# Performance work log

Hardware: AMD Instinct MI355X
Metric: run time of the kernel (lower is better)

## Reference

```python
import jax, jax.numpy as jnp
import numpy as np

NUM_SAMPLES = 1024


def _cdist(a, b):
    # a, b: (n, 3) -> (n, n) pairwise euclidean distances (torch.cdist p=2)
    d2 = jnp.sum((a[:, None, :] - b[None, :, :]) ** 2, axis=-1)
    return jnp.sqrt(jnp.maximum(d2, 0.0))


def _greedy_match_cost(cost):
    # Greedy sequential matching: repeatedly take the global argmin over
    # still-unmatched rows/cols, accumulate its cost, eliminate row+col.
    n = cost.shape[0]

    def step(carry, _):
        row_mask, col_mask, loss = carry
        valid = row_mask[:, None] & col_mask[None, :]
        masked = jnp.where(valid, cost, jnp.inf)
        idx = jnp.argmin(masked)  # row-major first-min == torch's min(dim=1)+argmin tiebreak
        r = idx // n
        c = idx % n
        loss = loss + cost[r, c]
        return (row_mask.at[r].set(False), col_mask.at[c].set(False), loss), None

    init = (jnp.ones((n,), dtype=bool), jnp.ones((n,), dtype=bool), jnp.float32(0.0))
    (_, _, loss), _ = jax.lax.scan(step, init, None, length=n)
    return loss / n


def setup_inputs() -> dict:
    key = jax.random.key(0)
    k1, k2, k3 = jax.random.split(key, 3)
    B, N, n = 8, 4096, NUM_SAMPLES
    S1 = jax.random.normal(k1, (B, N, 3), dtype=jnp.float32)
    S2 = jax.random.normal(k2, (B, N, 3), dtype=jnp.float32)
    # torch.randperm(N)[:n] per batch element: without-replacement sampling
    perm_keys = jax.random.split(k3, B)
    indices = jax.vmap(lambda k: jax.random.permutation(k, N)[:n])(perm_keys).astype(jnp.int32)
    return {"S1": S1, "S2": S2, "indices": indices}


def reference(S1, S2, indices):
    # sample the same indices from both sets, per batch (matches original loop)
    s1 = jnp.take_along_axis(S1, indices[:, :, None], axis=1)  # (B, n, 3)
    s2 = jnp.take_along_axis(S2, indices[:, :, None], axis=1)  # (B, n, 3)
    cost = jax.vmap(_cdist)(s1, s2)  # (B, n, n)
    losses = jax.vmap(_greedy_match_cost)(cost)  # (B,)
    return jnp.mean(losses)
```

## Files before the change

kernel.cpp:

```cpp
#include <hip/hip_runtime.h>
#include <stdint.h>

#define BATCH 8
#define NPTS 4096
#define NS 1024
#define KD 6

typedef unsigned long long u64;
typedef unsigned int u32;
typedef unsigned short u16;
typedef unsigned char u8;

#define DEADV (~0ull)
#define QNANB 0x7FC00000u

__device__ __forceinline__ float pdist3(float ax, float ay, float az,
                                        float bx, float by, float bz) {
    float dx = ax - bx, dy = ay - by, dz = az - bz;
    float d2 = __fmaf_rn(dz, dz, __fmaf_rn(dy, dy, dx * dx));
    return __fsqrt_rn(d2);
}

__device__ __forceinline__ u64 packv(float d, u32 row, u32 col) {
    return ((u64)__float_as_uint(d) << 20) | ((u64)row << 10) | (u64)col;
}

__device__ __forceinline__ u64 u64min2(u64 a, u64 b) { return a < b ? a : b; }
__device__ __forceinline__ u64 u64max2(u64 a, u64 b) { return a > b ? a : b; }

__device__ __forceinline__ u64 tree16(const u64* p) {
    u64 a0 = u64min2(p[0], p[1]),   a1 = u64min2(p[2], p[3]);
    u64 a2 = u64min2(p[4], p[5]),   a3 = u64min2(p[6], p[7]);
    u64 a4 = u64min2(p[8], p[9]),   a5 = u64min2(p[10], p[11]);
    u64 a6 = u64min2(p[12], p[13]), a7 = u64min2(p[14], p[15]);
    u64 b0 = u64min2(a0, a1), b1 = u64min2(a2, a3);
    u64 b2 = u64min2(a4, a5), b3 = u64min2(a6, a7);
    return u64min2(u64min2(b0, b1), u64min2(b2, b3));
}

template<int CTRL>
__device__ __forceinline__ u64 dpp_min_step(u64 m) {
    u32 lo = (u32)m, hi = (u32)(m >> 32);
    u32 olo = (u32)__builtin_amdgcn_update_dpp(-1, (int)lo, CTRL, 0xF, 0xF, false);
    u32 ohi = (u32)__builtin_amdgcn_update_dpp(-1, (int)hi, CTRL, 0xF, 0xF, false);
    u64 o = ((u64)ohi << 32) | olo;
    return o < m ? o : m;
}

__device__ __forceinline__ u64 wave_min_u64(u64 m) {
    m = dpp_min_step<0x111>(m);
    m = dpp_min_step<0x112>(m);
    m = dpp_min_step<0x114>(m);
    m = dpp_min_step<0x118>(m);
    m = dpp_min_step<0x142>(m);
    m = dpp_min_step<0x143>(m);
    u32 lo = (u32)__builtin_amdgcn_readlane((int)(u32)m, 63);
    u32 hi = (u32)__builtin_amdgcn_readlane((int)(u32)(m >> 32), 63);
    return ((u64)hi << 32) | lo;
}

__global__ void gather_k(const float* __restrict__ S1, const float* __restrict__ S2,
                         const int* __restrict__ idx,
                         float4* __restrict__ s1g, float4* __restrict__ s2g,
                         int* __restrict__ cnt) {
    int t = blockIdx.x * blockDim.x + threadIdx.x;
    if (t == 0) *cnt = 0;
    if (t >= BATCH * NS) return;
    int b = t >> 10;
    int j = idx[t];
    const float* p1 = S1 + ((size_t)b * NPTS + j) * 3;
    const float* p2 = S2 + ((size_t)b * NPTS + j) * 3;
    s1g[t] = make_float4(p1[0], p1[1], p1[2], 0.f);
    s2g[t] = make_float4(p2[0], p2[1], p2[2], 0.f);
}

__global__ void lists_k(const float4* __restrict__ s1g, const float4* __restrict__ s2g,
                        u64* __restrict__ rlist_g, u64* __restrict__ clist_g) {
    int gg = blockIdx.x * 4 + (threadIdx.x >> 6);
    int lane = threadIdx.x & 63;
    int side = (gg >= BATCH * NS) ? 1 : 0;
    int g = gg - side * (BATCH * NS);
    int b = g >> 10;
    u32 rc = (u32)(g & 1023);
    float4 a = side ? s2g[g] : s1g[g];
    const float4* other = (side ? s1g : s2g) + (size_t)b * NS;
    u64 cand[16];
    #pragma unroll
    for (int k = 0; k < 16; ++k) {
        int o = lane + (k << 6);
        float4 q = other[o];
        float d = pdist3(a.x, a.y, a.z, q.x, q.y, q.z);
        cand[k] = side ? packv(d, (u32)o, rc) : packv(d, rc, (u32)o);
    }
    u64* out = (side ? clist_g : rlist_g) + (size_t)g * KD;
    for (int i = 0; i < KD; ++i) {
        u64 m1 = wave_min_u64(tree16(cand));
        if (lane == 0) out[i] = m1;
        #pragma unroll
        for (int k = 0; k < 16; ++k) cand[k] = (cand[k] == m1) ? DEADV : cand[k];
    }
}

__global__ void __launch_bounds__(1024, 1)
resolve_k(const float4* __restrict__ s1g, const float4* __restrict__ s2g,
          const u64* __restrict__ rlist_gl, const u64* __restrict__ clist_gl,
          float* __restrict__ loss_ws, int* __restrict__ cnt,
          float* __restrict__ out) {
    __shared__ u64 rlist[NS * KD];
    __shared__ u64 clist[NS * KD];
    __shared__ u64 rmin[NS];
    __shared__ u64 cmin[NS];
    __shared__ float4 s1p[NS];
    __shared__ float4 s2p[NS];
    __shared__ u8 rptrs[NS], cptrs[NS];
    __shared__ u16 qrow[NS], qcol[NS];
    __shared__ u16 lrows[NS], lcols[NS];
    __shared__ float lred[1024];
    __shared__ int qrn, qcn, matched, nlr, nlc, stale_n;
    int b = blockIdx.x;
    int tid = threadIdx.x;
    int lane = tid & 63, wv = tid >> 6;

    {
        const float4* rs = (const float4*)(rlist_gl + (size_t)b * NS * KD);
        const float4* cs = (const float4*)(clist_gl + (size_t)b * NS * KD);
        float4* rd = (float4*)rlist;
        float4* cd = (float4*)clist;
        for (int i = tid; i < NS * KD / 2; i += 1024) { rd[i] = rs[i]; cd[i] = cs[i]; }
    }
    s1p[tid] = s1g[(size_t)b * NS + tid];
    s2p[tid] = s2g[(size_t)b * NS + tid];
    rptrs[tid] = 1; cptrs[tid] = 1;
    lrows[tid] = (u16)tid; lcols[tid] = (u16)tid;
    if (tid == 0) { matched = 0; stale_n = NS; }
    __syncthreads();
    rmin[tid] = rlist[tid * KD];
    cmin[tid] = clist[tid * KD];
    float loss = 0.f;
    __syncthreads();

    for (int round = 0; round < NS; ++round) {
        u64 myk = rmin[tid];
        u32 c = (u32)myk & 1023u;
        bool mut = (myk != DEADV) && (cmin[c] == myk);
        __syncthreads();
        if (mut) {
            loss += __uint_as_float((u32)(myk >> 20));
            rmin[tid] = DEADV;
            cmin[c] = DEADV;
            s1p[tid].x = __uint_as_float(QNANB);
            s2p[c].x   = __uint_as_float(QNANB);
        }
        u64 bal = __ballot((int)mut);
        if (lane == 0 && bal) atomicAdd(&matched, (int)__popcll(bal));
        if (tid == 0) { qrn = 0; qcn = 0; nlr = 0; nlc = 0; }
        __syncthreads();
        int m = matched;
        if (m >= NS) break;
        int live = NS - m;
        int stale = stale_n;
        bool rebuild = (stale * 4 > live * 5 + 64);
        u64 rk = rmin[tid];
        if (rk != DEADV) {
            float pr = s2p[(u32)rk & 1023u].x;
            if (pr != pr) {
                u32 p = rptrs[tid];
                bool found = false;
                while (p < KD) {
                    u64 e = rlist[tid * KD + p];
                    ++p;
                    if (e != DEADV) {
                        float q = s2p[(u32)e & 1023u].x;
                        if (q == q) { rmin[tid] = e; found = true; break; }
                    }
                }
                rptrs[tid] = (u8)p;
                if (!found) { int s = atomicAdd(&qrn, 1); qrow[s] = (u16)tid; }
            }
        }
        u64 ck = cmin[tid];
        if (ck != DEADV) {
            float pr = s1p[((u32)ck >> 10) & 1023u].x;
            if (pr != pr) {
                u32 p = cptrs[tid];
                bool found = false;
                while (p < KD) {
                    u64 e = clist[tid * KD + p];
                    ++p;
                    if (e != DEADV) {
                        float q = s1p[((u32)e >> 10) & 1023u].x;
                        if (q == q) { cmin[tid] = e; found = true; break; }
                    }
                }
                cptrs[tid] = (u8)p;
                if (!found) { int s = atomicAdd(&qcn, 1); qcol[s] = (u16)tid; }
            }
        }
        if (rebuild) {
            float cx = s2p[tid].x;
            bool calive = (cx == cx);
            u64 cb = __ballot((int)calive);
            int crank = (int)__popcll(cb & ((1ull << lane) - 1ull));
            int cbase = 0;
            if (lane == 0) cbase = atomicAdd(&nlc, (int)__popcll(cb));
            cbase = __shfl(cbase, 0, 64);
            if (calive) lcols[cbase + crank] = (u16)tid;

            float rx = s1p[tid].x;
            bool ralive = (rx == rx);
            u64 rb = __ballot((int)ralive);
            int rrank = (int)__popcll(rb & ((1ull << lane) - 1ull));
            int rbase = 0;
            if (lane == 0) rbase = atomicAdd(&nlr, (int)__popcll(rb));
            rbase = __shfl(rbase, 0, 64);
            if (ralive) lrows[rbase + rrank] = (u16)tid;
        }
        __syncthreads();
        int nr = qrn, nc = qcn;
        int scan_n = rebuild ? live : stale;
        if (rebuild && tid == 0) stale_n = live;
        for (int qi = wv; qi < nr; qi += 16) {
            u32 r = qrow[qi];
            float4 a = s1p[r];
            u64 m1 = DEADV, m2 = DEADV;
            for (int i = lane; i < scan_n; i += 64) {
                int cc = lcols[i];
                float4 q = s2p[cc];
                float d = pdist3(a.x, a.y, a.z, q.x, q.y, q.z);
                u64 p = packv(d, r, (u32)cc);
                u64 mx = u64max2(p, m1);
                m1 = u64min2(m1, p);
                m2 = u64min2(m2, mx);
            }
            u64 M1 = wave_min_u64(m1);
            u64 c2 = (m1 == M1) ? m2 : m1;
            u64 M2 = wave_min_u64(c2);
            if (lane == 0) {
                rmin[r] = M1;
                rlist[r * KD + KD - 1] = M2;
                rptrs[r] = KD - 1;
            }
        }
        for (int qi = wv; qi < nc; qi += 16) {
            u32 cc = qcol[qi];
            float4 a = s2p[cc];
            u64 m1 = DEADV, m2 = DEADV;
            for (int i = lane; i < scan_n; i += 64) {
                int r = lrows[i];
                float4 q = s1p[r];
                float d = pdist3(q.x, q.y, q.z, a.x, a.y, a.z);
                u64 p = packv(d, (u32)r, cc);
                u64 mx = u64max2(p, m1);
                m1 = u64min2(m1, p);
                m2 = u64min2(m2, mx);
            }
            u64 M1 = wave_min_u64(m1);
            u64 c2 = (m1 == M1) ? m2 : m1;
            u64 M2 = wave_min_u64(c2);
            if (lane == 0) {
                cmin[cc] = M1;
                clist[cc * KD + KD - 1] = M2;
                cptrs[cc] = KD - 1;
            }
        }
        __syncthreads();
    }

    lred[tid] = loss;
    __syncthreads();
    #pragma unroll
    for (int s = 512; s > 0; s >>= 1) {
        if (tid < s) lred[tid] += lred[tid + s];
        __syncthreads();
    }
    if (tid == 0) {
        atomicExch(&loss_ws[b], lred[0] * (1.0f / NS));
        __threadfence();
        int old = atomicAdd(cnt, 1);
        if (old == BATCH - 1) {
            __threadfence();
            float s = 0.f;
            for (int i = 0; i < BATCH; ++i) s += atomicAdd(&loss_ws[i], 0.0f);
            out[0] = s * (1.0f / BATCH);
        }
    }
}

extern "C" void kernel_launch(void* const* d_in, const int* in_sizes, int n_in,
                              void* d_out, int out_size, void* d_ws, size_t ws_size,
                              hipStream_t stream) {
    const float* S1 = (const float*)d_in[0];
    const float* S2 = (const float*)d_in[1];
    const int* idx  = (const int*)d_in[2];
    char* ws = (char*)d_ws;
    size_t o = 0;
    float4* s1g    = (float4*)(ws + o); o += (size_t)BATCH * NS * 16;
    float4* s2g    = (float4*)(ws + o); o += (size_t)BATCH * NS * 16;
    u64* rlist_g   = (u64*)(ws + o);    o += (size_t)BATCH * NS * KD * 8;
    u64* clist_g   = (u64*)(ws + o);    o += (size_t)BATCH * NS * KD * 8;
    float* loss_ws = (float*)(ws + o);  o += (size_t)BATCH * 4;
    int* cnt       = (int*)(ws + o);

    gather_k<<<(BATCH * NS + 255) / 256, 256, 0, stream>>>(S1, S2, idx, s1g, s2g, cnt);
    lists_k<<<2 * BATCH * NS / 4, 256, 0, stream>>>(s1g, s2g, rlist_g, clist_g);
    resolve_k<<<BATCH, 1024, 0, stream>>>(s1g, s2g, rlist_g, clist_g, loss_ws, cnt,
                                          (float*)d_out);
}
```

Before: 198.8 us.

## Merge row/column rescans, use float top-2 tracking, stage points in LDS

The separate row and column rescan loops are merged into one work list spread over all 16 waves, so unbalanced row/col queues no longer leave waves idle. The inner top-2 tracking now compares 32-bit floats with indices instead of packed 64-bit keys, and the key is only built after the wave reduction. The rebuild compaction replaces LDS atomics with a per-wave count prefix, at the cost of an extra barrier. lists_k stages the partner point set in shared memory instead of reading it from global memory in every wave.

Result: no change. 201.0 us (+1.1%).

```diff
diff --git a/kernel.cpp b/kernel.cpp
--- a/kernel.cpp
+++ b/kernel.cpp
@@ -13,6 +13,7 @@
 
 #define DEADV (~0ull)
 #define QNANB 0x7FC00000u
+#define INFB  0x7F800000u
 
 __device__ __forceinline__ float pdist3(float ax, float ay, float az,
                                         float bx, float by, float bz) {
@@ -26,7 +27,6 @@
 }
 
 __device__ __forceinline__ u64 u64min2(u64 a, u64 b) { return a < b ? a : b; }
-__device__ __forceinline__ u64 u64max2(u64 a, u64 b) { return a > b ? a : b; }
 
 __device__ __forceinline__ u64 tree16(const u64* p) {
     u64 a0 = u64min2(p[0], p[1]),   a1 = u64min2(p[2], p[3]);
@@ -76,19 +76,22 @@
 
 __global__ void lists_k(const float4* __restrict__ s1g, const float4* __restrict__ s2g,
                         u64* __restrict__ rlist_g, u64* __restrict__ clist_g) {
+    __shared__ float4 pts[NS];
     int gg = blockIdx.x * 4 + (threadIdx.x >> 6);
     int lane = threadIdx.x & 63;
     int side = (gg >= BATCH * NS) ? 1 : 0;
     int g = gg - side * (BATCH * NS);
     int b = g >> 10;
     u32 rc = (u32)(g & 1023);
+    const float4* other = (side ? s1g : s2g) + (size_t)b * NS;
+    for (int i = threadIdx.x; i < NS; i += 256) pts[i] = other[i];
     float4 a = side ? s2g[g] : s1g[g];
-    const float4* other = (side ? s1g : s2g) + (size_t)b * NS;
+    __syncthreads();
     u64 cand[16];
     #pragma unroll
     for (int k = 0; k < 16; ++k) {
         int o = lane + (k << 6);
-        float4 q = other[o];
+        float4 q = pts[o];
         float d = pdist3(a.x, a.y, a.z, q.x, q.y, q.z);
         cand[k] = side ? packv(d, (u32)o, rc) : packv(d, rc, (u32)o);
     }
@@ -116,7 +119,8 @@
     __shared__ u16 qrow[NS], qcol[NS];
     __shared__ u16 lrows[NS], lcols[NS];
     __shared__ float lred[1024];
-    __shared__ int qrn, qcn, matched, nlr, nlc, stale_n;
+    __shared__ int wcntr[16], wcntc[16];
+    __shared__ int qrn, qcn, matched, stale_n;
     int b = blockIdx.x;
     int tid = threadIdx.x;
     int lane = tid & 63, wv = tid >> 6;
@@ -153,7 +157,7 @@
         }
         u64 bal = __ballot((int)mut);
         if (lane == 0 && bal) atomicAdd(&matched, (int)__popcll(bal));
-        if (tid == 0) { qrn = 0; qcn = 0; nlr = 0; nlc = 0; }
+        if (tid == 0) { qrn = 0; qcn = 0; }
         __syncthreads();
         int m = matched;
         if (m >= NS) break;
@@ -197,70 +201,83 @@
             }
         }
         if (rebuild) {
-            float cx = s2p[tid].x;
-            bool calive = (cx == cx);
+            float cx = s2p[tid].x;  bool calive = (cx == cx);
+            float rx = s1p[tid].x;  bool ralive = (rx == rx);
             u64 cb = __ballot((int)calive);
+            u64 rb = __ballot((int)ralive);
+            if (lane == 0) { wcntc[wv] = (int)__popcll(cb); wcntr[wv] = (int)__popcll(rb); }
+            __syncthreads();
+            int cbase = 0, rbase = 0;
+            for (int j = 0; j < wv; ++j) { cbase += wcntc[j]; rbase += wcntr[j]; }
             int crank = (int)__popcll(cb & ((1ull << lane) - 1ull));
-            int cbase = 0;
-            if (lane == 0) cbase = atomicAdd(&nlc, (int)__popcll(cb));
-            cbase = __shfl(cbase, 0, 64);
+            int rrank = (int)__popcll(rb & ((1ull << lane) - 1ull));
             if (calive) lcols[cbase + crank] = (u16)tid;
-
-            float rx = s1p[tid].x;
-            bool ralive = (rx == rx);
-            u64 rb = __ballot((int)ralive);
-            int rrank = (int)__popcll(rb & ((1ull << lane) - 1ull));
-            int rbase = 0;
-            if (lane == 0) rbase = atomicAdd(&nlr, (int)__popcll(rb));
-            rbase = __shfl(rbase, 0, 64);
             if (ralive) lrows[rbase + rrank] = (u16)tid;
         }
         __syncthreads();
         int nr = qrn, nc = qcn;
         int scan_n = rebuild ? live : stale;
         if (rebuild && tid == 0) stale_n = live;
-        for (int qi = wv; qi < nr; qi += 16) {
-            u32 r = qrow[qi];
-            float4 a = s1p[r];
-            u64 m1 = DEADV, m2 = DEADV;
-            for (int i = lane; i < scan_n; i += 64) {
-                int cc = lcols[i];
-                float4 q = s2p[cc];
-                float d = pdist3(a.x, a.y, a.z, q.x, q.y, q.z);
-                u64 p = packv(d, r, (u32)cc);
-                u64 mx = u64max2(p, m1);
-                m1 = u64min2(m1, p);
-                m2 = u64min2(m2, mx);
-            }
-            u64 M1 = wave_min_u64(m1);
-            u64 c2 = (m1 == M1) ? m2 : m1;
-            u64 M2 = wave_min_u64(c2);
-            if (lane == 0) {
-                rmin[r] = M1;
-                rlist[r * KD + KD - 1] = M2;
-                rptrs[r] = KD - 1;
-            }
-        }
-        for (int qi = wv; qi < nc; qi += 16) {
-            u32 cc = qcol[qi];
-            float4 a = s2p[cc];
-            u64 m1 = DEADV, m2 = DEADV;
-            for (int i = lane; i < scan_n; i += 64) {
-                int r = lrows[i];
-                float4 q = s1p[r];
-                float d = pdist3(q.x, q.y, q.z, a.x, a.y, a.z);
-                u64 p = packv(d, (u32)r, cc);
-                u64 mx = u64max2(p, m1);
-                m1 = u64min2(m1, p);
-                m2 = u64min2(m2, mx);
-            }
-            u64 M1 = wave_min_u64(m1);
-            u64 c2 = (m1 == M1) ? m2 : m1;
-            u64 M2 = wave_min_u64(c2);
-            if (lane == 0) {
-                cmin[cc] = M1;
-                clist[cc * KD + KD - 1] = M2;
-                cptrs[cc] = KD - 1;
+        int tot = nr + nc;
+        for (int qi = wv; qi < tot; qi += 16) {
+            if (qi < nr) {
+                u32 r = qrow[qi];
+                float4 a = s1p[r];
+                float a1d = __uint_as_float(INFB), a2d = a1d;
+                u32 a1i = 1023u, a2i = 1023u;
+                for (int i = lane; i < scan_n; i += 64) {
+                    int cc = lcols[i];
+                    float4 q = s2p[cc];
+                    float d = pdist3(a.x, a.y, a.z, q.x, q.y, q.z);
+                    bool c1 = d < a1d;
+                    bool c2 = d < a2d;
+                    float td = c2 ? d : a2d;  u32 ti = c2 ? (u32)cc : a2i;
+                    a2d = c1 ? a1d : td;      a2i = c1 ? a1i : ti;
+                    a1d = c1 ? d : a1d;       a1i = c1 ? (u32)cc : a1i;
+                }
+                u32 b1 = __float_as_uint(a1d), b2 = __float_as_uint(a2d);
+                u64 m1 = (b1 == INFB) ? DEADV : (((u64)b1 << 10) | a1i);
+                u64 m2 = (b2 == INFB) ? DEADV : (((u64)b2 << 10) | a2i);
+                u64 M1 = wave_min_u64(m1);
+                u64 ck2 = (m1 == M1) ? m2 : m1;
+                u64 M2 = wave_min_u64(ck2);
+                if (lane == 0) {
+                    u64 F1 = ((M1 >> 10) << 20) | ((u64)r << 10) | (M1 & 1023u);
+                    u64 F2 = (M2 == DEADV) ? DEADV
+                           : (((M2 >> 10) << 20) | ((u64)r << 10) | (M2 & 1023u));
+                    rmin[r] = F1;
+                    rlist[r * KD + KD - 1] = F2;
+                    rptrs[r] = KD - 1;
+                }
+            } else {
+                u32 cc = qcol[qi - nr];
+                float4 a = s2p[cc];
+                float a1d = __uint_as_float(INFB), a2d = a1d;
+                u32 a1i = 1023u, a2i = 1023u;
+                for (int i = lane; i < scan_n; i += 64) {
+                    int r = lrows[i];
+                    float4 q = s1p[r];
+                    float d = pdist3(q.x, q.y, q.z, a.x, a.y, a.z);
+                    bool c1 = d < a1d;
+                    bool c2 = d < a2d;
+                    float td = c2 ? d : a2d;  u32 ti = c2 ? (u32)r : a2i;
+                    a2d = c1 ? a1d : td;      a2i = c1 ? a1i : ti;
+                    a1d = c1 ? d : a1d;       a1i = c1 ? (u32)r : a1i;
+                }
+                u32 b1 = __float_as_uint(a1d), b2 = __float_as_uint(a2d);
+                u64 m1 = (b1 == INFB) ? DEADV : (((u64)b1 << 10) | a1i);
+                u64 m2 = (b2 == INFB) ? DEADV : (((u64)b2 << 10) | a2i);
+                u64 M1 = wave_min_u64(m1);
+                u64 ck2 = (m1 == M1) ? m2 : m1;
+                u64 M2 = wave_min_u64(ck2);
+                if (lane == 0) {
+                    u64 F1 = ((M1 >> 10) << 20) | ((M1 & 1023u) << 10) | (u64)cc;
+                    u64 F2 = (M2 == DEADV) ? DEADV
+                           : (((M2 >> 10) << 20) | ((M2 & 1023u) << 10) | (u64)cc);
+                    cmin[cc] = F1;
+                    clist[cc * KD + KD - 1] = F2;
+                    cptrs[cc] = KD - 1;
+                }
             }
         }
         __syncthreads();
```
